# Kernel tuning notes

Measured on AMD Instinct MI355X. Metric: run time of the kernel, lower is better.

Reference implementation:

```python
import jax, jax.numpy as jnp
import numpy as np

HEADS = 16
DIM_HEAD = 64
SCALE = DIM_HEAD ** -0.5


def setup_inputs() -> dict:
    key = jax.random.key(0)
    k1, k2, k3, k4 = jax.random.split(key, 4)
    b, n, dim = 2, 2048, 1024
    inner = HEADS * DIM_HEAD  # 1024
    x = jax.random.normal(k1, (b, n, dim), dtype=jnp.float32)
    # binary keep-mask (multiplicative, as in the original module)
    seq_mask = (jax.random.uniform(k2, (b, n)) < 0.9).astype(jnp.float32)
    # weights stored [in, out] (transpose of torch Linear layout)
    w_qkv = jax.random.normal(k3, (dim, inner * 3), dtype=jnp.float32) * (dim ** -0.5)
    w_out = jax.random.normal(k4, (inner, dim), dtype=jnp.float32) * (inner ** -0.5)
    return {"x": x, "seq_mask": seq_mask, "w_qkv": w_qkv, "w_out": w_out}


def reference(x, seq_mask, w_qkv, w_out):
    b, n, dim = x.shape
    qkv = x @ w_qkv                                   # [b, n, 3*inner]
    q, k, v = jnp.split(qkv, 3, axis=-1)
    split_heads = lambda t: t.reshape(b, n, HEADS, DIM_HEAD).transpose(0, 2, 1, 3)
    q, k, v = split_heads(q), split_heads(k), split_heads(v)  # [b, h, n, d]
    dots = jnp.einsum('bhid,bhjd->bhij', q, k) * SCALE        # [b, h, n, n]
    # multiplicative mask, broadcast over heads and query index i; mask depends on key index j
    dots = dots * seq_mask[:, None, None, :]
    attn = jax.nn.softmax(dots, axis=-1)
    out = jnp.einsum('bhij,bhjd->bhid', attn, v)              # [b, h, n, d]
    out = out.transpose(0, 2, 1, 3).reshape(b, n, HEADS * DIM_HEAD)
    return out @ w_out                                        # dropout p=0 -> identity
```

## Files before the change

### kernel.cpp

```cpp
#include <hip/hip_runtime.h>
#include <hip/hip_bf16.h>

using bf16 = __hip_bfloat16;
typedef __attribute__((ext_vector_type(8))) short short8;
typedef __attribute__((ext_vector_type(4))) float floatx4;

#define MFMA_BF16(a, b, c) __builtin_amdgcn_mfma_f32_16x16x32_bf16((a), (b), (c), 0, 0, 0)

__device__ __forceinline__ void gload_lds16(const bf16* g, bf16* l) {
  __builtin_amdgcn_global_load_lds((__attribute__((address_space(1))) void*)g,
                                   (__attribute__((address_space(3))) void*)l,
                                   16, 0, 0);
}

__device__ __forceinline__ unsigned short bfbits(float f) {
  bf16 b = __float2bfloat16(f);
  return *reinterpret_cast<unsigned short*>(&b);
}

__global__ __launch_bounds__(256)
void probemask_k(const void* __restrict__ msrc, bf16* __restrict__ dst,
                 int* __restrict__ flag) {
  __shared__ int any;
  const int tid = threadIdx.x;
  if (tid == 0) any = 0;
  __syncthreads();
  const unsigned* mw = (const unsigned*)msrc;
  int bad = 0;
#pragma unroll
  for (int i = 0; i < 4; i++) {
    unsigned w = mw[tid * 4 + i];
    if (w != 0u && w != 0x3F800000u) bad = 1;
  }
  if (bad) atomicOr(&any, 1);
  __syncthreads();
  const int isbf = any;
  if (tid == 0) flag[0] = isbf;
  if (isbf) {
#pragma unroll
    for (int i = 0; i < 2; i++)
      ((int4*)dst)[tid * 2 + i] = ((const int4*)msrc)[tid * 2 + i];
  } else {
#pragma unroll
    for (int i = 0; i < 4; i++) {
      float4 v = ((const float4*)msrc)[tid * 4 + i];
      int o = tid * 16 + i * 4;
      dst[o + 0] = __float2bfloat16(v.x);
      dst[o + 1] = __float2bfloat16(v.y);
      dst[o + 2] = __float2bfloat16(v.z);
      dst[o + 3] = __float2bfloat16(v.w);
    }
  }
}

__global__ __launch_bounds__(256)
void cvt_k(const void* __restrict__ src, bf16* __restrict__ dst, int n,
           const int* __restrict__ flag) {
  if (*flag) return;
  int i = (blockIdx.x * 256 + threadIdx.x) * 4;
  if (i >= n) return;
  float4 v = ((const float4*)src)[i >> 2];
  dst[i + 0] = __float2bfloat16(v.x);
  dst[i + 1] = __float2bfloat16(v.y);
  dst[i + 2] = __float2bfloat16(v.z);
  dst[i + 3] = __float2bfloat16(v.w);
}

__global__ __launch_bounds__(256)
void transpose2_k(const void* __restrict__ in0, bf16* __restrict__ out0,
                  const void* __restrict__ in1, bf16* __restrict__ out1,
                  const int* __restrict__ flag) {
  __shared__ bf16 tile[32][33];
  const int isbf = *flag;
  constexpr int R = 1024;
  const void* in;
  bf16* out;
  int C, bx;
  if (blockIdx.x < 96) { in = in0; out = out0; C = 3072; bx = blockIdx.x * 32; }
  else                 { in = in1; out = out1; C = 1024; bx = (blockIdx.x - 96) * 32; }
  int by = blockIdx.y * 32;
  int tx = threadIdx.x & 31, ty = threadIdx.x >> 5;
#pragma unroll
  for (int i = 0; i < 4; i++) {
    size_t idx = (size_t)(by + ty + i * 8) * C + bx + tx;
    tile[ty + i * 8][tx] =
        isbf ? ((const bf16*)in)[idx] : __float2bfloat16(((const float*)in)[idx]);
  }
  __syncthreads();
#pragma unroll
  for (int i = 0; i < 4; i++)
    out[(size_t)(bx + ty + i * 8) * R + by + tx] = tile[tx][ty + i * 8];
}

template <int MODE>
__global__ __launch_bounds__(256, 2)
void gemm_k(const bf16* __restrict__ A, const bf16* __restrict__ Aalt,
            const bf16* __restrict__ Bt,
            bf16* __restrict__ Qo, bf16* __restrict__ Ko, bf16* __restrict__ Vo,
            void* __restrict__ Co, const bf16* __restrict__ Mk,
            const int* __restrict__ flag) {
  constexpr int K = 1024;
  __shared__ __align__(16) bf16 As[128 * 32];
  __shared__ __align__(16) bf16 Bs[128 * 32];

  const int tid = threadIdx.x;
  const int lane = tid & 63;
  const int wv = tid >> 6;
  const int wm = wv & 1, wn = wv >> 1;
  const int l15 = lane & 15, quad = lane >> 4;

  const int bm = blockIdx.y * 128;
  const int bn = blockIdx.x * 128;

  const int sml = tid >> 2;
  const int sg = (tid & 3) ^ ((sml >> 1) & 3);

  const bf16* Ab = (MODE == 0 && *flag) ? Aalt : A;

  floatx4 acc[4][4] = {};

  for (int k0 = 0; k0 < K; k0 += 32) {
    __syncthreads();
    const bf16 *a0, *a1;
    if (MODE == 0) {
      a0 = Ab + (size_t)(bm + sml) * K + k0 + sg * 8;
      a1 = a0 + (size_t)64 * K;
    } else {
      const int b_idx = bm >> 11;
      const int h = k0 >> 6;
      const int d = (k0 & 63) + sg * 8;
      const int nn = bm & 2047;
      const bf16* base = Ab + (size_t)(b_idx * 16 + h) * 131072 + d;
      a0 = base + (size_t)(nn + sml) * 64;
      a1 = base + (size_t)(nn + 64 + sml) * 64;
    }
    gload_lds16(a0, &As[tid * 8]);
    gload_lds16(a1, &As[2048 + tid * 8]);
    const bf16* b0 = Bt + (size_t)(bn + sml) * K + k0 + sg * 8;
    gload_lds16(b0, &Bs[tid * 8]);
    gload_lds16(b0 + (size_t)64 * K, &Bs[2048 + tid * 8]);
    __syncthreads();

    short8 af[4], bfr[4];
#pragma unroll
    for (int mi = 0; mi < 4; mi++) {
      int m = wm * 64 + mi * 16 + l15;
      af[mi] = *(const short8*)&As[m * 32 + ((quad ^ ((m >> 1) & 3)) * 8)];
    }
#pragma unroll
    for (int ni = 0; ni < 4; ni++) {
      int n = wn * 64 + ni * 16 + l15;
      bfr[ni] = *(const short8*)&Bs[n * 32 + ((quad ^ ((n >> 1) & 3)) * 8)];
    }
#pragma unroll
    for (int mi = 0; mi < 4; mi++)
#pragma unroll
      for (int ni = 0; ni < 4; ni++)
        acc[mi][ni] = MFMA_BF16(af[mi], bfr[ni], acc[mi][ni]);
  }

  const int isbf = (MODE == 1) ? *flag : 0;

#pragma unroll
  for (int mi = 0; mi < 4; mi++) {
    const int row0 = bm + wm * 64 + mi * 16 + quad * 4;
#pragma unroll
    for (int ni = 0; ni < 4; ni++) {
      const int col = bn + wn * 64 + ni * 16 + l15;
      if (MODE == 0) {
        const int sec = col >> 10;
        const int cc = col & 1023;
        const int h = cc >> 6, d = cc & 63;
        const int b_idx = row0 >> 11;
        const int nn0 = row0 & 2047;
        if (sec == 0) {
          bf16* dst = Qo + (size_t)(b_idx * 16 + h) * 131072 + (size_t)nn0 * 64 + d;
#pragma unroll
          for (int r = 0; r < 4; r++) dst[r * 64] = __float2bfloat16(acc[mi][ni][r]);
        } else if (sec == 1) {
          const bf16* mrow = Mk + (size_t)b_idx * 2048 + nn0;
          bf16* dst = Ko + (size_t)(b_idx * 16 + h) * 131072 + (size_t)nn0 * 64 + d;
#pragma unroll
          for (int r = 0; r < 4; r++)
            dst[r * 64] = __float2bfloat16(acc[mi][ni][r] * 0.125f *
                                           __bfloat162float(mrow[r]));
        } else {
          bf16* dst = Vo + (size_t)(b_idx * 16 + h) * 131072 + (size_t)d * 2048 + nn0;
#pragma unroll
          for (int r = 0; r < 4; r++) dst[r] = __float2bfloat16(acc[mi][ni][r]);
        }
      } else {
        if (isbf) {
          bf16* C2 = (bf16*)Co;
#pragma unroll
          for (int r = 0; r < 4; r++)
            C2[(size_t)(row0 + r) * 1024 + col] = __float2bfloat16(acc[mi][ni][r]);
        } else {
          float* C2 = (float*)Co;
#pragma unroll
          for (int r = 0; r < 4; r++)
            C2[(size_t)(row0 + r) * 1024 + col] = acc[mi][ni][r];
        }
      }
    }
  }
}

__global__ __launch_bounds__(256, 4)
void flash_k(const bf16* __restrict__ Q, const bf16* __restrict__ K,
             const bf16* __restrict__ VT, bf16* __restrict__ O) {
  __shared__ __align__(16) bf16 Ks[2][4096];
  __shared__ __align__(16) bf16 Vs[2][4096];
  __shared__ __align__(16) bf16 Ps[4096];

  const int tid = threadIdx.x;
  const int lane = tid & 63;
  const int w = tid >> 6;
  const int l15 = lane & 15, quad = lane >> 4;
  const int sw7 = l15 & 7;

  const int qt = blockIdx.x & 31;
  const int hl = blockIdx.x >> 5;

  const bf16* Qh = Q + (size_t)hl * 131072;
  const bf16* Kh = K + (size_t)hl * 131072;
  const bf16* Vh = VT + (size_t)hl * 131072;
  bf16* Oh = O + (size_t)hl * 131072;

  const int qrow = qt * 64 + w * 16;
  short8 qf[2];
#pragma unroll
  for (int kk = 0; kk < 2; kk++)
    qf[kk] = *(const short8*)&Qh[(size_t)(qrow + l15) * 64 + kk * 32 + quad * 8];

  floatx4 o_acc[4] = {};
  float rsum = 0.f;

  bf16* Psw = Ps + w * 1024;

  const int sjj = tid >> 3;
  const int sgp = (tid & 7) ^ (sjj & 7);

  gload_lds16(&Kh[(size_t)sjj * 64 + sgp * 8], &Ks[0][tid * 8]);
  gload_lds16(&Kh[(size_t)(32 + sjj) * 64 + sgp * 8], &Ks[0][2048 + tid * 8]);
  gload_lds16(&Vh[(size_t)sjj * 2048 + sgp * 8], &Vs[0][tid * 8]);
  gload_lds16(&Vh[(size_t)(32 + sjj) * 2048 + sgp * 8], &Vs[0][2048 + tid * 8]);

  for (int it = 0; it < 32; ++it) {
    const int b = it & 1;
    __syncthreads();
    if (it < 31) {
      const int j1 = (it + 1) * 64;
      gload_lds16(&Kh[(size_t)(j1 + sjj) * 64 + sgp * 8], &Ks[b ^ 1][tid * 8]);
      gload_lds16(&Kh[(size_t)(j1 + 32 + sjj) * 64 + sgp * 8], &Ks[b ^ 1][2048 + tid * 8]);
      gload_lds16(&Vh[(size_t)sjj * 2048 + j1 + sgp * 8], &Vs[b ^ 1][tid * 8]);
      gload_lds16(&Vh[(size_t)(32 + sjj) * 2048 + j1 + sgp * 8], &Vs[b ^ 1][2048 + tid * 8]);
    }

    floatx4 s[4] = {};
#pragma unroll
    for (int nj = 0; nj < 4; nj++) {
      const int jj = nj * 16 + l15;
#pragma unroll
      for (int kk = 0; kk < 2; kk++) {
        const int gk = kk * 4 + quad;
        short8 kf = *(const short8*)&Ks[b][jj * 64 + ((gk ^ (jj & 7)) * 8)];
        s[nj] = MFMA_BF16(kf, qf[kk], s[nj]);
      }
    }

    float rs = 0.f;
#pragma unroll
    for (int nj = 0; nj < 4; nj++)
#pragma unroll
      for (int r = 0; r < 4; r++) {
        const float p = __expf(s[nj][r]);
        s[nj][r] = p;
        rs += p;
      }
    rs += __shfl_xor(rs, 16, 64);
    rs += __shfl_xor(rs, 32, 64);
    rsum += rs;

#pragma unroll
    for (int nj = 0; nj < 4; nj++) {
      ushort4 u;
      u.x = bfbits(s[nj][0]);
      u.y = bfbits(s[nj][1]);
      u.z = bfbits(s[nj][2]);
      u.w = bfbits(s[nj][3]);
      const int G = nj * 2 + (quad >> 1), h = quad & 1;
      *(ushort4*)&Psw[l15 * 64 + ((G ^ sw7) * 8) + h * 4] = u;
    }
    __builtin_amdgcn_wave_barrier();

    short8 pf[2];
#pragma unroll
    for (int kk = 0; kk < 2; kk++)
      pf[kk] = *(const short8*)&Psw[l15 * 64 + (((kk * 4 + quad) ^ sw7) * 8)];

#pragma unroll
    for (int ni = 0; ni < 4; ni++) {
      const int dd = ni * 16 + l15;
#pragma unroll
      for (int kk = 0; kk < 2; kk++) {
        const int gk = kk * 4 + quad;
        short8 vf = *(const short8*)&Vs[b][dd * 64 + ((gk ^ (dd & 7)) * 8)];
        o_acc[ni] = MFMA_BF16(pf[kk], vf, o_acc[ni]);
      }
    }
  }

  float rinv[4];
#pragma unroll
  for (int r = 0; r < 4; r++)
    rinv[r] = 1.f / __shfl(rsum, quad * 4 + r, 64);
#pragma unroll
  for (int ni = 0; ni < 4; ni++) {
    const int d = ni * 16 + l15;
#pragma unroll
    for (int r = 0; r < 4; r++) {
      const int row = qrow + quad * 4 + r;
      Oh[(size_t)row * 64 + d] = __float2bfloat16(o_acc[ni][r] * rinv[r]);
    }
  }
}

extern "C" void kernel_launch(void* const* d_in, const int* in_sizes, int n_in,
                              void* d_out, int out_size, void* d_ws, size_t ws_size,
                              hipStream_t stream) {
  const void* x     = d_in[0];
  const void* mask  = d_in[1];
  const void* w_qkv = d_in[2];
  const void* w_out = d_in[3];

  bf16* ws    = (bf16*)d_ws;
  bf16* xb    = ws;
  bf16* AO    = ws;
  bf16* wqkvT = ws + 4194304;
  bf16* woutT = wqkvT + 3145728;
  bf16* Qb    = woutT + 1048576;
  bf16* Kb    = Qb + 4194304;
  bf16* maskb = Kb + 4194304;
  int*  flag  = (int*)(maskb + 4096);
  bf16* VT    = (bf16*)d_out;

  probemask_k<<<1, 256, 0, stream>>>(mask, maskb, flag);
  cvt_k<<<4096, 256, 0, stream>>>(x, xb, 4194304, flag);
  transpose2_k<<<dim3(128, 32), 256, 0, stream>>>(w_qkv, wqkvT, w_out, woutT, flag);
  gemm_k<0><<<dim3(24, 32), 256, 0, stream>>>(xb, (const bf16*)x, wqkvT, Qb, Kb, VT,
                                              nullptr, maskb, flag);
  flash_k<<<1024, 256, 0, stream>>>(Qb, Kb, VT, AO);
  gemm_k<1><<<dim3(8, 32), 256, 0, stream>>>(AO, nullptr, woutT, nullptr, nullptr,
                                             nullptr, d_out, nullptr, flag);
}
```

Measured before the change: 202.0 us.

## Fuse prep kernels, widen flash wave tiles, use exp2 scaling, retile out-proj GEMM

Merges the mask probe, x conversion and weight transposes into one prep kernel, and each kernel now derives the dtype flag itself with a wave ballot, which removes two launches and the flag buffer. The flash kernel runs 128 threads per block, and each wave handles two 16-row query sets that share K and V fragment loads. It folds log2(e) into the K scaling so it can call exp2f and writes output with vectorized stores. The output GEMM uses a 64-wide N tile to launch more blocks. The risks are lower occupancy or more register pressure in flash and redundant mask reads in every block.

```diff
diff --git a/kernel.cpp b/kernel.cpp
--- a/kernel.cpp
+++ b/kernel.cpp
@@ -18,90 +18,90 @@
   return *reinterpret_cast<unsigned short*>(&b);
 }
 
+__device__ __forceinline__ bool derive_isbf(const unsigned* __restrict__ rawmask,
+                                            int lane) {
+  int bad = 0;
+#pragma unroll
+  for (int i = 0; i < 8; i++) {
+    unsigned v = rawmask[lane * 8 + i];
+    if (v != 0u && v != 0x3F800000u) bad = 1;
+  }
+  return __ballot(bad) != 0ull;
+}
+
+#define KSCALE 0.18033688011112042f
+
 __global__ __launch_bounds__(256)
-void probemask_k(const void* __restrict__ msrc, bf16* __restrict__ dst,
-                 int* __restrict__ flag) {
-  __shared__ int any;
+void prep_k(const void* __restrict__ x, const void* __restrict__ w_qkv,
+            const void* __restrict__ w_out, const unsigned* __restrict__ rawmask,
+            bf16* __restrict__ xb, bf16* __restrict__ wqkvT,
+            bf16* __restrict__ woutT, bf16* __restrict__ maskb) {
+  __shared__ bf16 tile[32][33];
   const int tid = threadIdx.x;
-  if (tid == 0) any = 0;
-  __syncthreads();
-  const unsigned* mw = (const unsigned*)msrc;
-  int bad = 0;
-#pragma unroll
-  for (int i = 0; i < 4; i++) {
-    unsigned w = mw[tid * 4 + i];
-    if (w != 0u && w != 0x3F800000u) bad = 1;
-  }
-  if (bad) atomicOr(&any, 1);
-  __syncthreads();
-  const int isbf = any;
-  if (tid == 0) flag[0] = isbf;
-  if (isbf) {
-#pragma unroll
-    for (int i = 0; i < 2; i++)
-      ((int4*)dst)[tid * 2 + i] = ((const int4*)msrc)[tid * 2 + i];
+  const bool isbf = derive_isbf(rawmask, tid & 63);
+  const int bid = blockIdx.x;
+
+  if (bid < 4096) {
+    const void* in;
+    bf16* out;
+    int C, bx, by;
+    if (bid < 3072) {
+      in = w_qkv; out = wqkvT; C = 3072;
+      bx = (bid % 96) * 32; by = (bid / 96) * 32;
+    } else {
+      const int l = bid - 3072;
+      in = w_out; out = woutT; C = 1024;
+      bx = (l % 32) * 32; by = (l / 32) * 32;
+    }
+    const int tx = tid & 31, ty = tid >> 5;
+#pragma unroll
+    for (int i = 0; i < 4; i++) {
+      size_t idx = (size_t)(by + ty + i * 8) * C + bx + tx;
+      tile[ty + i * 8][tx] =
+          isbf ? ((const bf16*)in)[idx] : __float2bfloat16(((const float*)in)[idx]);
+    }
+    __syncthreads();
+#pragma unroll
+    for (int i = 0; i < 4; i++)
+      out[(size_t)(bx + ty + i * 8) * 1024 + by + tx] = tile[tx][ty + i * 8];
+  } else if (bid < 8192) {
+    if (isbf) return;
+    const int i = ((bid - 4096) * 256 + tid) * 4;
+    float4 v = ((const float4*)x)[i >> 2];
+    xb[i + 0] = __float2bfloat16(v.x);
+    xb[i + 1] = __float2bfloat16(v.y);
+    xb[i + 2] = __float2bfloat16(v.z);
+    xb[i + 3] = __float2bfloat16(v.w);
   } else {
-#pragma unroll
-    for (int i = 0; i < 4; i++) {
-      float4 v = ((const float4*)msrc)[tid * 4 + i];
-      int o = tid * 16 + i * 4;
-      dst[o + 0] = __float2bfloat16(v.x);
-      dst[o + 1] = __float2bfloat16(v.y);
-      dst[o + 2] = __float2bfloat16(v.z);
-      dst[o + 3] = __float2bfloat16(v.w);
-    }
-  }
-}
-
-__global__ __launch_bounds__(256)
-void cvt_k(const void* __restrict__ src, bf16* __restrict__ dst, int n,
-           const int* __restrict__ flag) {
-  if (*flag) return;
-  int i = (blockIdx.x * 256 + threadIdx.x) * 4;
-  if (i >= n) return;
-  float4 v = ((const float4*)src)[i >> 2];
-  dst[i + 0] = __float2bfloat16(v.x);
-  dst[i + 1] = __float2bfloat16(v.y);
-  dst[i + 2] = __float2bfloat16(v.z);
-  dst[i + 3] = __float2bfloat16(v.w);
-}
-
-__global__ __launch_bounds__(256)
-void transpose2_k(const void* __restrict__ in0, bf16* __restrict__ out0,
-                  const void* __restrict__ in1, bf16* __restrict__ out1,
-                  const int* __restrict__ flag) {
-  __shared__ bf16 tile[32][33];
-  const int isbf = *flag;
-  constexpr int R = 1024;
-  const void* in;
-  bf16* out;
-  int C, bx;
-  if (blockIdx.x < 96) { in = in0; out = out0; C = 3072; bx = blockIdx.x * 32; }
-  else                 { in = in1; out = out1; C = 1024; bx = (blockIdx.x - 96) * 32; }
-  int by = blockIdx.y * 32;
-  int tx = threadIdx.x & 31, ty = threadIdx.x >> 5;
-#pragma unroll
-  for (int i = 0; i < 4; i++) {
-    size_t idx = (size_t)(by + ty + i * 8) * C + bx + tx;
-    tile[ty + i * 8][tx] =
-        isbf ? ((const bf16*)in)[idx] : __float2bfloat16(((const float*)in)[idx]);
-  }
-  __syncthreads();
-#pragma unroll
-  for (int i = 0; i < 4; i++)
-    out[(size_t)(bx + ty + i * 8) * R + by + tx] = tile[tx][ty + i * 8];
-}
-
-template <int MODE>
+    if (isbf) {
+#pragma unroll
+      for (int i = 0; i < 2; i++)
+        ((int4*)maskb)[tid * 2 + i] = ((const int4*)rawmask)[tid * 2 + i];
+    } else {
+#pragma unroll
+      for (int i = 0; i < 4; i++) {
+        float4 v = ((const float4*)rawmask)[tid * 4 + i];
+        const int o = tid * 16 + i * 4;
+        maskb[o + 0] = __float2bfloat16(v.x);
+        maskb[o + 1] = __float2bfloat16(v.y);
+        maskb[o + 2] = __float2bfloat16(v.z);
+        maskb[o + 3] = __float2bfloat16(v.w);
+      }
+    }
+  }
+}
+
+template <int MODE, int BN>
 __global__ __launch_bounds__(256, 2)
 void gemm_k(const bf16* __restrict__ A, const bf16* __restrict__ Aalt,
             const bf16* __restrict__ Bt,
             bf16* __restrict__ Qo, bf16* __restrict__ Ko, bf16* __restrict__ Vo,
             void* __restrict__ Co, const bf16* __restrict__ Mk,
-            const int* __restrict__ flag) {
+            const unsigned* __restrict__ rawmask) {
   constexpr int K = 1024;
+  constexpr int NI = BN / 32;
   __shared__ __align__(16) bf16 As[128 * 32];
-  __shared__ __align__(16) bf16 Bs[128 * 32];
+  __shared__ __align__(16) bf16 Bs[BN * 32];
 
   const int tid = threadIdx.x;
   const int lane = tid & 63;
@@ -110,14 +110,15 @@
   const int l15 = lane & 15, quad = lane >> 4;
 
   const int bm = blockIdx.y * 128;
-  const int bn = blockIdx.x * 128;
+  const int bn = blockIdx.x * BN;
 
   const int sml = tid >> 2;
   const int sg = (tid & 3) ^ ((sml >> 1) & 3);
 
-  const bf16* Ab = (MODE == 0 && *flag) ? Aalt : A;
-
-  floatx4 acc[4][4] = {};
+  const bool isbf = derive_isbf(rawmask, lane);
+  const bf16* Ab = (MODE == 0 && isbf) ? Aalt : A;
+
+  floatx4 acc[4][NI] = {};
 
   for (int k0 = 0; k0 < K; k0 += 32) {
     __syncthreads();
@@ -137,36 +138,35 @@
     gload_lds16(a0, &As[tid * 8]);
     gload_lds16(a1, &As[2048 + tid * 8]);
     const bf16* b0 = Bt + (size_t)(bn + sml) * K + k0 + sg * 8;
-    gload_lds16(b0, &Bs[tid * 8]);
-    gload_lds16(b0 + (size_t)64 * K, &Bs[2048 + tid * 8]);
+#pragma unroll
+    for (int bi = 0; bi < BN / 64; bi++)
+      gload_lds16(b0 + (size_t)(bi * 64) * K, &Bs[bi * 2048 + tid * 8]);
     __syncthreads();
 
-    short8 af[4], bfr[4];
+    short8 af[4], bfr[NI];
 #pragma unroll
     for (int mi = 0; mi < 4; mi++) {
       int m = wm * 64 + mi * 16 + l15;
       af[mi] = *(const short8*)&As[m * 32 + ((quad ^ ((m >> 1) & 3)) * 8)];
     }
 #pragma unroll
-    for (int ni = 0; ni < 4; ni++) {
-      int n = wn * 64 + ni * 16 + l15;
+    for (int ni = 0; ni < NI; ni++) {
+      int n = wn * (BN / 2) + ni * 16 + l15;
       bfr[ni] = *(const short8*)&Bs[n * 32 + ((quad ^ ((n >> 1) & 3)) * 8)];
     }
 #pragma unroll
     for (int mi = 0; mi < 4; mi++)
 #pragma unroll
-      for (int ni = 0; ni < 4; ni++)
+      for (int ni = 0; ni < NI; ni++)
         acc[mi][ni] = MFMA_BF16(af[mi], bfr[ni], acc[mi][ni]);
   }
-
-  const int isbf = (MODE == 1) ? *flag : 0;
 
 #pragma unroll
   for (int mi = 0; mi < 4; mi++) {
     const int row0 = bm + wm * 64 + mi * 16 + quad * 4;
 #pragma unroll
-    for (int ni = 0; ni < 4; ni++) {
-      const int col = bn + wn * 64 + ni * 16 + l15;
+    for (int ni = 0; ni < NI; ni++) {
+      const int col = bn + wn * (BN / 2) + ni * 16 + l15;
       if (MODE == 0) {
         const int sec = col >> 10;
         const int cc = col & 1023;
@@ -182,7 +182,7 @@
           bf16* dst = Ko + (size_t)(b_idx * 16 + h) * 131072 + (size_t)nn0 * 64 + d;
 #pragma unroll
           for (int r = 0; r < 4; r++)
-            dst[r * 64] = __float2bfloat16(acc[mi][ni][r] * 0.125f *
+            dst[r * 64] = __float2bfloat16(acc[mi][ni][r] * KSCALE *
                                            __bfloat162float(mrow[r]));
         } else {
           bf16* dst = Vo + (size_t)(b_idx * 16 + h) * 131072 + (size_t)d * 2048 + nn0;
@@ -206,7 +206,7 @@
   }
 }
 
-__global__ __launch_bounds__(256, 4)
+__global__ __launch_bounds__(128, 2)
 void flash_k(const bf16* __restrict__ Q, const bf16* __restrict__ K,
              const bf16* __restrict__ VT, bf16* __restrict__ O) {
   __shared__ __align__(16) bf16 Ks[2][4096];
@@ -227,101 +227,118 @@
   const bf16* Vh = VT + (size_t)hl * 131072;
   bf16* Oh = O + (size_t)hl * 131072;
 
-  const int qrow = qt * 64 + w * 16;
-  short8 qf[2];
-#pragma unroll
-  for (int kk = 0; kk < 2; kk++)
-    qf[kk] = *(const short8*)&Qh[(size_t)(qrow + l15) * 64 + kk * 32 + quad * 8];
-
-  floatx4 o_acc[4] = {};
-  float rsum = 0.f;
-
-  bf16* Psw = Ps + w * 1024;
+  const int qbase = qt * 64 + w * 32;
+  short8 qf[2][2];
+#pragma unroll
+  for (int set = 0; set < 2; set++)
+#pragma unroll
+    for (int kk = 0; kk < 2; kk++)
+      qf[set][kk] =
+          *(const short8*)&Qh[(size_t)(qbase + set * 16 + l15) * 64 + kk * 32 + quad * 8];
+
+  floatx4 o_acc[2][4] = {};
+  float rsum[2] = {0.f, 0.f};
+
+  bf16* Psw = Ps + w * 2048;
 
   const int sjj = tid >> 3;
   const int sgp = (tid & 7) ^ (sjj & 7);
 
-  gload_lds16(&Kh[(size_t)sjj * 64 + sgp * 8], &Ks[0][tid * 8]);
-  gload_lds16(&Kh[(size_t)(32 + sjj) * 64 + sgp * 8], &Ks[0][2048 + tid * 8]);
-  gload_lds16(&Vh[(size_t)sjj * 2048 + sgp * 8], &Vs[0][tid * 8]);
-  gload_lds16(&Vh[(size_t)(32 + sjj) * 2048 + sgp * 8], &Vs[0][2048 + tid * 8]);
+#pragma unroll
+  for (int i = 0; i < 4; i++) {
+    gload_lds16(&Kh[(size_t)(i * 16 + sjj) * 64 + sgp * 8], &Ks[0][i * 1024 + tid * 8]);
+    gload_lds16(&Vh[(size_t)(i * 16 + sjj) * 2048 + sgp * 8], &Vs[0][i * 1024 + tid * 8]);
+  }
 
   for (int it = 0; it < 32; ++it) {
     const int b = it & 1;
     __syncthreads();
     if (it < 31) {
       const int j1 = (it + 1) * 64;
-      gload_lds16(&Kh[(size_t)(j1 + sjj) * 64 + sgp * 8], &Ks[b ^ 1][tid * 8]);
-      gload_lds16(&Kh[(size_t)(j1 + 32 + sjj) * 64 + sgp * 8], &Ks[b ^ 1][2048 + tid * 8]);
-      gload_lds16(&Vh[(size_t)sjj * 2048 + j1 + sgp * 8], &Vs[b ^ 1][tid * 8]);
-      gload_lds16(&Vh[(size_t)(32 + sjj) * 2048 + j1 + sgp * 8], &Vs[b ^ 1][2048 + tid * 8]);
-    }
-
-    floatx4 s[4] = {};
+#pragma unroll
+      for (int i = 0; i < 4; i++) {
+        gload_lds16(&Kh[(size_t)(j1 + i * 16 + sjj) * 64 + sgp * 8],
+                    &Ks[b ^ 1][i * 1024 + tid * 8]);
+        gload_lds16(&Vh[(size_t)(i * 16 + sjj) * 2048 + j1 + sgp * 8],
+                    &Vs[b ^ 1][i * 1024 + tid * 8]);
+      }
+    }
+
+    floatx4 s[2][4] = {};
 #pragma unroll
     for (int nj = 0; nj < 4; nj++) {
       const int jj = nj * 16 + l15;
 #pragma unroll
       for (int kk = 0; kk < 2; kk++) {
-        const int gk = kk * 4 + quad;
-        short8 kf = *(const short8*)&Ks[b][jj * 64 + ((gk ^ (jj & 7)) * 8)];
-        s[nj] = MFMA_BF16(kf, qf[kk], s[nj]);
-      }
-    }
-
-    float rs = 0.f;
-#pragma unroll
-    for (int nj = 0; nj < 4; nj++)
-#pragma unroll
-      for (int r = 0; r < 4; r++) {
-        const float p = __expf(s[nj][r]);
-        s[nj][r] = p;
-        rs += p;
-      }
-    rs += __shfl_xor(rs, 16, 64);
-    rs += __shfl_xor(rs, 32, 64);
-    rsum += rs;
-
-#pragma unroll
-    for (int nj = 0; nj < 4; nj++) {
-      ushort4 u;
-      u.x = bfbits(s[nj][0]);
-      u.y = bfbits(s[nj][1]);
-      u.z = bfbits(s[nj][2]);
-      u.w = bfbits(s[nj][3]);
-      const int G = nj * 2 + (quad >> 1), h = quad & 1;
-      *(ushort4*)&Psw[l15 * 64 + ((G ^ sw7) * 8) + h * 4] = u;
-    }
-    __builtin_amdgcn_wave_barrier();
-
-    short8 pf[2];
-#pragma unroll
-    for (int kk = 0; kk < 2; kk++)
-      pf[kk] = *(const short8*)&Psw[l15 * 64 + (((kk * 4 + quad) ^ sw7) * 8)];
-
+        short8 kf = *(const short8*)&Ks[b][jj * 64 + (((kk * 4 + quad) ^ (jj & 7)) * 8)];
+        s[0][nj] = MFMA_BF16(kf, qf[0][kk], s[0][nj]);
+        s[1][nj] = MFMA_BF16(kf, qf[1][kk], s[1][nj]);
+      }
+    }
+
+    short8 vf[4][2];
 #pragma unroll
     for (int ni = 0; ni < 4; ni++) {
       const int dd = ni * 16 + l15;
 #pragma unroll
-      for (int kk = 0; kk < 2; kk++) {
-        const int gk = kk * 4 + quad;
-        short8 vf = *(const short8*)&Vs[b][dd * 64 + ((gk ^ (dd & 7)) * 8)];
-        o_acc[ni] = MFMA_BF16(pf[kk], vf, o_acc[ni]);
-      }
-    }
-  }
-
-  float rinv[4];
-#pragma unroll
-  for (int r = 0; r < 4; r++)
-    rinv[r] = 1.f / __shfl(rsum, quad * 4 + r, 64);
-#pragma unroll
-  for (int ni = 0; ni < 4; ni++) {
-    const int d = ni * 16 + l15;
-#pragma unroll
-    for (int r = 0; r < 4; r++) {
-      const int row = qrow + quad * 4 + r;
-      Oh[(size_t)row * 64 + d] = __float2bfloat16(o_acc[ni][r] * rinv[r]);
+      for (int kk = 0; kk < 2; kk++)
+        vf[ni][kk] =
+            *(const short8*)&Vs[b][dd * 64 + (((kk * 4 + quad) ^ (dd & 7)) * 8)];
+    }
+
+#pragma unroll
+    for (int set = 0; set < 2; set++) {
+      float rs = 0.f;
+#pragma unroll
+      for (int nj = 0; nj < 4; nj++)
+#pragma unroll
+        for (int r = 0; r < 4; r++) {
+          const float p = exp2f(s[set][nj][r]);
+          s[set][nj][r] = p;
+          rs += p;
+        }
+      rs += __shfl_xor(rs, 16, 64);
+      rs += __shfl_xor(rs, 32, 64);
+      rsum[set] += rs;
+
+      const int prow = set * 16 + l15;
+#pragma unroll
+      for (int nj = 0; nj < 4; nj++) {
+        ushort4 u;
+        u.x = bfbits(s[set][nj][0]);
+        u.y = bfbits(s[set][nj][1]);
+        u.z = bfbits(s[set][nj][2]);
+        u.w = bfbits(s[set][nj][3]);
+        const int G = nj * 2 + (quad >> 1);
+        *(ushort4*)&Psw[prow * 64 + ((G ^ sw7) * 8) + (quad & 1) * 4] = u;
+      }
+      __builtin_amdgcn_wave_barrier();
+
+      short8 pf[2];
+#pragma unroll
+      for (int kk = 0; kk < 2; kk++)
+        pf[kk] = *(const short8*)&Psw[prow * 64 + (((kk * 4 + quad) ^ sw7) * 8)];
+
+#pragma unroll
+      for (int ni = 0; ni < 4; ni++)
+#pragma unroll
+        for (int kk = 0; kk < 2; kk++)
+          o_acc[set][ni] = MFMA_BF16(vf[ni][kk], pf[kk], o_acc[set][ni]);
+    }
+  }
+
+#pragma unroll
+  for (int set = 0; set < 2; set++) {
+    const float rinv = 1.f / rsum[set];
+    const size_t row = (size_t)(qbase + set * 16 + l15) * 64;
+#pragma unroll
+    for (int ni = 0; ni < 4; ni++) {
+      ushort4 u;
+      u.x = bfbits(o_acc[set][ni][0] * rinv);
+      u.y = bfbits(o_acc[set][ni][1] * rinv);
+      u.z = bfbits(o_acc[set][ni][2] * rinv);
+      u.w = bfbits(o_acc[set][ni][3] * rinv);
+      *(ushort4*)&Oh[row + ni * 16 + quad * 4] = u;
     }
   }
 }
@@ -342,15 +359,14 @@
   bf16* Qb    = woutT + 1048576;
   bf16* Kb    = Qb + 4194304;
   bf16* maskb = Kb + 4194304;
-  int*  flag  = (int*)(maskb + 4096);
   bf16* VT    = (bf16*)d_out;
 
-  probemask_k<<<1, 256, 0, stream>>>(mask, maskb, flag);
-  cvt_k<<<4096, 256, 0, stream>>>(x, xb, 4194304, flag);
-  transpose2_k<<<dim3(128, 32), 256, 0, stream>>>(w_qkv, wqkvT, w_out, woutT, flag);
-  gemm_k<0><<<dim3(24, 32), 256, 0, stream>>>(xb, (const bf16*)x, wqkvT, Qb, Kb, VT,
-                                              nullptr, maskb, flag);
-  flash_k<<<1024, 256, 0, stream>>>(Qb, Kb, VT, AO);
-  gemm_k<1><<<dim3(8, 32), 256, 0, stream>>>(AO, nullptr, woutT, nullptr, nullptr,
-                                             nullptr, d_out, nullptr, flag);
-}
+  prep_k<<<8193, 256, 0, stream>>>(x, w_qkv, w_out, (const unsigned*)mask,
+                                   xb, wqkvT, woutT, maskb);
+  gemm_k<0, 128><<<dim3(24, 32), 256, 0, stream>>>(
+      xb, (const bf16*)x, wqkvT, Qb, Kb, VT, nullptr, maskb, (const unsigned*)mask);
+  flash_k<<<1024, 128, 0, stream>>>(Qb, Kb, VT, AO);
+  gemm_k<1, 64><<<dim3(16, 32), 256, 0, stream>>>(
+      AO, nullptr, woutT, nullptr, nullptr, nullptr, d_out, nullptr,
+      (const unsigned*)mask);
+}
```

After: 232.0 us. 14.9% more time.
